# Optimization experiments

Hardware: AMD Instinct MI355X
Metric: run time of the kernel (lower is better)

Reference implementation:

```python
import jax, jax.numpy as jnp
import numpy as np

N_QUBITS = 12
R = 1
EDGES = [(i, (i + 1) % N_QUBITS) for i in range(N_QUBITS)]
DIM = 2 ** N_QUBITS
BATCH = 64
_LET = 'abcdefghijklmnopqrstuvwxy'

_I4 = np.eye(4, dtype=np.float32)
_AD = np.fliplr(_I4).copy()                      # antidiagonal (XX imag pattern)
_YP = np.array([[0,0,0,1],[0,0,-1,0],[0,-1,0,0],[1,0,0,0]], dtype=np.float32)  # YY imag pattern
_CNOT = jnp.asarray(np.array([[1,0,0,0],[0,1,0,0],[0,0,0,1],[0,0,1,0]], dtype=np.complex64))
_k = np.arange(DIM)
# z_signs[i, k] = -1 if bit (n-i-1) of k is set, matching the torch buffer
_ZS = jnp.asarray(np.stack([1.0 - 2.0 * ((_k >> (N_QUBITS - i - 1)) & 1) for i in range(N_QUBITS)]).astype(np.float32))  # [n, 2^n]


def _c(r, i):
    return jax.lax.complex(r, i)


def rx_mat(t):
    c, s, z = jnp.cos(t / 2), jnp.sin(t / 2), jnp.zeros_like(t)
    real = jnp.stack([jnp.stack([c, z], -1), jnp.stack([z, c], -1)], -2)
    imag = jnp.stack([jnp.stack([z, -s], -1), jnp.stack([-s, z], -1)], -2)
    return _c(real, imag)


def ry_mat(t):
    c, s = jnp.cos(t / 2), jnp.sin(t / 2)
    real = jnp.stack([jnp.stack([c, -s], -1), jnp.stack([s, c], -1)], -2)
    return _c(real, jnp.zeros_like(real))


def rz_mat(t):
    p, z = t / 2, jnp.zeros_like(t)
    cp, sp = jnp.cos(p), jnp.sin(p)
    real = jnp.stack([jnp.stack([cp, z], -1), jnp.stack([z, cp], -1)], -2)
    imag = jnp.stack([jnp.stack([-sp, z], -1), jnp.stack([z, sp], -1)], -2)
    return _c(real, imag)


def ising_zz(t):
    p = t / 2
    c, s = jnp.cos(p), jnp.sin(p)
    dr = jnp.stack([c, c, c, c], -1)
    di = jnp.stack([-s, s, s, -s], -1)
    i4 = jnp.asarray(_I4)
    return _c(dr[..., :, None] * i4, di[..., :, None] * i4)


def ising_xx(t):
    c, s = jnp.cos(t / 2), jnp.sin(t / 2)
    return _c(c[..., None, None] * jnp.asarray(_I4), -s[..., None, None] * jnp.asarray(_AD))


def ising_yy(t):
    c, s = jnp.cos(t / 2), jnp.sin(t / 2)
    return _c(c[..., None, None] * jnp.asarray(_I4), s[..., None, None] * jnp.asarray(_YP))


def apply_1q(state, gate, q):
    # state [B, 2^n]; gate [2,2] or [B,2,2]; qubit axis sits at stride 2^q (matches torch view)
    B = state.shape[0]
    left, right = 2 ** (N_QUBITS - q - 1), 2 ** q
    s = state.reshape(B, left, 2, right)
    sub = 'bij' if gate.ndim == 3 else 'ij'
    return jnp.einsum(f'{sub},bljr->blir', gate, s).reshape(B, DIM)


def apply_2q(state, gate, q1, q2):
    # state [B, 2^n]; gate [4,4]; qubit index = tensor-axis index from MSB (matches torch permute path)
    if q1 > q2:
        q1, q2 = q2, q1
    B = state.shape[0]
    s = state.reshape((B,) + (2,) * N_QUBITS)
    g = gate.reshape(2, 2, 2, 2)
    ax = list(_LET[:N_QUBITS])
    out = ax.copy()
    u, v = ax[q1], ax[q2]
    out[q1], out[q2] = 'A', 'B'
    spec = f"AB{u}{v},Z{''.join(ax)}->Z{''.join(out)}"
    return jnp.einsum(spec, g, s).reshape(B, DIM)


def _forward(data, encoding_scale, encoding_bias, eta, ew_zz, ew_xx, ew_yy, nb_z, nb_x, nb_y, trainable_rots):
    B, n = data.shape
    # data-encoding gates, cached once per forward: angles [B, n] -> gates [B, n, 2, 2]
    rx_g = rx_mat(encoding_scale[:, 0] * data + encoding_bias[:, 0])
    ry_g = ry_mat(encoding_scale[:, 1] * data + encoding_bias[:, 1])
    rz_g = rz_mat(encoding_scale[:, 2] * data + encoding_bias[:, 2])
    state = jnp.zeros((B, DIM), jnp.complex64).at[:, 0].set(1.0)
    ising_fns = (ising_zz, ising_xx, ising_yy)
    ews = (ew_zz, ew_xx, ew_yy)
    nbs = (nb_z, nb_x, nb_y)
    bias_fns = (rz_mat, rx_mat, ry_mat)
    enc_types = ('full', 'xy', 'yz')
    for r in range(R):
        for b in range(3):  # blocks: ZZ, XX, YY
            bt = enc_types[b]
            # data encoding
            for q in range(n):
                if bt != 'yz':
                    state = apply_1q(state, rx_g[:, q], q)
                state = apply_1q(state, ry_g[:, q], q)
                if bt != 'xy':
                    state = apply_1q(state, rz_g[:, q], q)
            # Ising interaction on each edge
            theta = eta[r, b] * ews[b][r]            # [n_edges]
            egs = ising_fns[b](theta)                # [n_edges, 4, 4]
            for e, (i, j) in enumerate(EDGES):
                state = apply_2q(state, egs[e], i, j)
            # node biases (RZ / RX / RY matching the block)
            bgs = bias_fns[b](nbs[b][r])             # [n, 2, 2]
            for q in range(n):
                state = apply_1q(state, bgs[q], q)
            # trainable rotations rx, ry, rz per qubit
            rots = trainable_rots[r, b]              # [n, 3]
            rxg, ryg, rzg = rx_mat(rots[:, 0]), ry_mat(rots[:, 1]), rz_mat(rots[:, 2])
            for q in range(n):
                state = apply_1q(state, rxg[q], q)
                state = apply_1q(state, ryg[q], q)
                state = apply_1q(state, rzg[q], q)
            # CNOT entangling ring
            for q in range(n):
                state = apply_2q(state, _CNOT, q, (q + 1) % n)
    probs = state.real ** 2 + state.imag ** 2        # [B, 2^n]
    return probs @ _ZS.T                             # Pauli-Z expectations [B, n]


def setup_inputs() -> dict:
    key = jax.random.key(0)
    ks = jax.random.split(key, 12)
    n, E, f = N_QUBITS, len(EDGES), jnp.float32
    return {
        'data': jax.random.uniform(ks[0], (BATCH, n), f),
        'encoding_scale': jnp.pi * jnp.ones((n, 3), f) + 0.1 * jax.random.normal(ks[1], (n, 3), f),
        'encoding_bias': 0.1 * jax.random.normal(ks[2], (n, 3), f),
        'eta': 0.5 * jnp.ones((R, 3), f),
        'ew_zz': jnp.ones((R, E), f) + 0.1 * jax.random.normal(ks[3], (R, E), f),
        'ew_xx': jnp.ones((R, E), f) + 0.1 * jax.random.normal(ks[4], (R, E), f),
        'ew_yy': jnp.ones((R, E), f) + 0.1 * jax.random.normal(ks[5], (R, E), f),
        'nb_z': 0.1 * jax.random.normal(ks[6], (R, n), f),
        'nb_x': 0.1 * jax.random.normal(ks[7], (R, n), f),
        'nb_y': 0.1 * jax.random.normal(ks[8], (R, n), f),
        'trainable_rots': 0.1 * jax.random.normal(ks[9], (R, 3, n, 3), f),
    }


def reference(data, encoding_scale, encoding_bias, eta, ew_zz, ew_xx, ew_yy, nb_z, nb_x, nb_y, trainable_rots):
    return _forward(data, encoding_scale, encoding_bias, eta, ew_zz, ew_xx, ew_yy, nb_z, nb_x, nb_y, trainable_rots)
```

## Files before the change

kernel.cpp:

```cpp
#include <hip/hip_runtime.h>
#include <math.h>

#define NT 512
#define QDIM 4096

typedef float v2f __attribute__((ext_vector_type(2)));
using F2 = float2;

__device__ __forceinline__ v2f mkv(float x, float y) { v2f r; r.x = x; r.y = y; return r; }

__device__ __forceinline__ v2f cfma(v2f m, v2f a, v2f acc) {
    v2f r;
    asm("v_pk_fma_f32 %0, %1, %2, %3 op_sel:[0,0,0] op_sel_hi:[0,1,1]\n\t"
        "v_pk_fma_f32 %0, %1, %2, %0 op_sel:[1,1,0] op_sel_hi:[1,0,1] neg_lo:[1,0,0]"
        : "=&v"(r) : "v"(m), "v"(a), "v"(acc));
    return r;
}
__device__ __forceinline__ v2f cmulp(v2f m, v2f a) {
    v2f r;
    asm("v_pk_mul_f32 %0, %1, %2 op_sel:[0,0] op_sel_hi:[0,1]\n\t"
        "v_pk_fma_f32 %0, %1, %2, %0 op_sel:[1,1,0] op_sel_hi:[1,0,1] neg_lo:[1,0,0]"
        : "=&v"(r) : "v"(m), "v"(a));
    return r;
}

__device__ __forceinline__ F2 cadd(F2 p, F2 q) { return make_float2(p.x + q.x, p.y + q.y); }
__device__ __forceinline__ F2 cmul(F2 p, F2 q) {
    return make_float2(p.x * q.x - p.y * q.y, p.x * q.y + p.y * q.x);
}
struct M2 { F2 a, b, c, d; };
__device__ __forceinline__ M2 mmul(M2 A, M2 B) {
    M2 R;
    R.a = cadd(cmul(A.a, B.a), cmul(A.b, B.c));
    R.b = cadd(cmul(A.a, B.b), cmul(A.b, B.d));
    R.c = cadd(cmul(A.c, B.a), cmul(A.d, B.c));
    R.d = cadd(cmul(A.c, B.b), cmul(A.d, B.d));
    return R;
}
__device__ __forceinline__ M2 mrx(float t) {
    float s, c; sincosf(0.5f * t, &s, &c);
    return { make_float2(c, 0), make_float2(0, -s), make_float2(0, -s), make_float2(c, 0) };
}
__device__ __forceinline__ M2 mry(float t) {
    float s, c; sincosf(0.5f * t, &s, &c);
    return { make_float2(c, 0), make_float2(-s, 0), make_float2(s, 0), make_float2(c, 0) };
}
__device__ __forceinline__ M2 mrz(float t) {
    float s, c; sincosf(0.5f * t, &s, &c);
    return { make_float2(c, -s), make_float2(0, 0), make_float2(0, 0), make_float2(c, s) };
}
#define RSQ2 0.70710678118654752f
__device__ __forceinline__ M2 mH() {
    return { make_float2(RSQ2, 0), make_float2(RSQ2, 0), make_float2(RSQ2, 0), make_float2(-RSQ2, 0) };
}
__device__ __forceinline__ M2 mW() {
    return { make_float2(RSQ2, 0), make_float2(0, RSQ2), make_float2(RSQ2, 0), make_float2(0, -RSQ2) };
}
__device__ __forceinline__ M2 mWd() {
    return { make_float2(RSQ2, 0), make_float2(RSQ2, 0), make_float2(0, -RSQ2), make_float2(0, RSQ2) };
}


template<int Li>
__device__ __forceinline__ int kOf(int t, int j) {
    const int mlo = (1 << (3 * Li)) - 1;
    return (t & mlo) | (j << (3 * Li)) | ((t & ~mlo) << 3);
}
__device__ __forceinline__ int slot0(int k) {
    int j = k & 7, t = k >> 3;
    return j * 512 + (t ^ j);
}

template<int TYPE>
__device__ __forceinline__ void itrip(v2f* amp, int l, v2f* wb) {
#pragma unroll
    for (int j = 0; j < 8; ++j) wb[j * 64 + (l ^ ((9 * j) & 63))] = amp[j];
    asm volatile("" ::: "memory");
#pragma unroll
    for (int j = 0; j < 8; ++j) {
        int jo, lo;
        if (TYPE == 0) { jo = l & 7;        lo = j | (l & 56); }
        else           { jo = (l >> 3) & 7; lo = (l & 7) | (j << 3); }
        amp[j] = wb[jo * 64 + (lo ^ ((9 * jo) & 63))];
    }
}

__device__ __forceinline__ void btrip(v2f* amp, int tid, int l, int wv, v2f* b) {
#pragma unroll
    for (int j = 0; j < 8; ++j) b[j * 512 + (tid ^ j)] = amp[j];
    __syncthreads();
#pragma unroll
    for (int j = 0; j < 8; ++j) amp[j] = b[wv * 512 + ((j * 64 + l) ^ wv)];
}

struct Trio { v2f m[12]; };
__device__ __forceinline__ Trio load_trio(const float4 (*g4)[2]) {
    Trio t;
#pragma unroll
    for (int k = 0; k < 3; ++k) {
        float4 a = g4[k][0], b = g4[k][1];
        t.m[k * 4 + 0] = mkv(a.x, a.y); t.m[k * 4 + 1] = mkv(a.z, a.w);
        t.m[k * 4 + 2] = mkv(b.x, b.y); t.m[k * 4 + 3] = mkv(b.z, b.w);
    }
    return t;
}

template<int JB>
__device__ __forceinline__ void g1_reg(v2f* amp, const v2f* g) {
    const int m = 1 << JB;
    v2f m00 = g[0], m01 = g[1], m10 = g[2], m11 = g[3];
#pragma unroll
    for (int j = 0; j < 8; ++j)
        if (!(j & m)) {
            v2f a = amp[j], b = amp[j | m];
            amp[j]     = cfma(m01, b, cmulp(m00, a));
            amp[j | m] = cfma(m11, b, cmulp(m10, a));
        }
}
__device__ __forceinline__ void apply_trio(v2f* amp, const Trio& t) {
    g1_reg<0>(amp, t.m + 0);  g1_reg<1>(amp, t.m + 4);  g1_reg<2>(amp, t.m + 8);
}

__device__ __forceinline__ void diag_L3(v2f* amp, const float* zh, int tid) {
    float phi0 = 0.f;
#pragma unroll
    for (int e = 3; e <= 10; ++e) {
        int hi = 11 - e, lo = 10 - e;
        phi0 += (((tid >> hi) ^ (tid >> lo)) & 1) ? zh[e] : -zh[e];
    }
    float z0 = zh[0], z1 = zh[1], z2 = zh[2], z11 = zh[11];
    int t8 = (tid >> 8) & 1, t0 = tid & 1;
#pragma unroll
    for (int j = 0; j < 8; ++j) {
        int j0 = j & 1, j1 = (j >> 1) & 1, j2 = (j >> 2) & 1;
        float phi = phi0
            + ((j2 ^ j1) ? z0 : -z0)
            + ((j1 ^ j0) ? z1 : -z1)
            + ((j0 ^ t8) ? z2 : -z2)
            + ((j2 ^ t0) ? z11 : -z11);
        float sp, cp;
        __sincosf(phi, &sp, &cp);
        amp[j] = cmulp(mkv(cp, sp), amp[j]);
    }
}

__device__ __forceinline__ int cnot_src(int k) {
#pragma unroll
    for (int e = 11; e >= 0; --e) {
        int hi = (e < 11) ? 11 - e : 11, lo = (e < 11) ? 10 - e : 0;
        if ((k >> hi) & 1) k ^= (1 << lo);
    }
    return k;
}

__device__ __forceinline__ void cnot_pair(v2f* amp, int tid, int l, int pw, int gen,
                                          const int* kslot, v2f* b,
                                          volatile unsigned* wflag, int wv) {
#pragma unroll
    for (int j = 0; j < 8; ++j) b[j * 512 + (tid ^ j)] = amp[j];
    asm volatile("" ::: "memory");
    __threadfence_block();
    if (l == 0) wflag[wv] = (unsigned)gen;
    asm volatile("" ::: "memory");
    int guard = 0;
    while (wflag[pw] < (unsigned)gen && guard < (1 << 26)) {
        ++guard;
        __builtin_amdgcn_s_sleep(1);
    }
    asm volatile("" ::: "memory");
#pragma unroll
    for (int j = 0; j < 8; ++j) amp[j] = b[kslot[j]];
}

__global__ __launch_bounds__(NT) void qsim_kernel(
    const float* __restrict__ data,
    const float* __restrict__ enc_scale,
    const float* __restrict__ enc_bias,
    const float* __restrict__ eta,
    const float* __restrict__ ew_zz,
    const float* __restrict__ ew_xx,
    const float* __restrict__ ew_yy,
    const float* __restrict__ nb_z,
    const float* __restrict__ nb_x,
    const float* __restrict__ nb_y,
    const float* __restrict__ trots,
    float* __restrict__ out)
{
    __shared__ v2f bbuf[2][QDIM];
    __shared__ v2f ibuf[QDIM];
    __shared__ float4 g1q4[72][2];
    __shared__ float zhalf[3][12];
    __shared__ float red[8][12];
    __shared__ unsigned wflag[8];

    const int tid = threadIdx.x;
    const int l = tid & 63, wv = tid >> 6;
    const int bat = blockIdx.x;
    v2f* wb = &ibuf[wv * 512];

    if (tid < 36) {
        int b = tid / 12, q = tid % 12;
        float x  = data[bat * 12 + q];
        float ax = enc_scale[q * 3 + 0] * x + enc_bias[q * 3 + 0];
        float ay = enc_scale[q * 3 + 1] * x + enc_bias[q * 3 + 1];
        float az = enc_scale[q * 3 + 2] * x + enc_bias[q * 3 + 2];
        M2 M;
        if (b == 0)      M = mmul(mrz(az), mmul(mry(ay), mrx(ax)));
        else if (b == 1) M = mmul(mH(), mmul(mry(ay), mrx(ax)));
        else             M = mmul(mW(), mmul(mrz(az), mry(ay)));
        g1q4[tid][0] = make_float4(M.a.x, M.a.y, M.b.x, M.b.y);
        g1q4[tid][1] = make_float4(M.c.x, M.c.y, M.d.x, M.d.y);
    } else if (tid < 72) {
        int i = tid - 36, b = i / 12, q = i % 12;
        float nb = (b == 0) ? nb_z[q] : (b == 1) ? nb_x[q] : nb_y[q];
        M2 M0 = (b == 0) ? mrz(nb) : (b == 1) ? mrx(nb) : mry(nb);
        float t0 = trots[(b * 12 + q) * 3 + 0];
        float t1 = trots[(b * 12 + q) * 3 + 1];
        float t2 = trots[(b * 12 + q) * 3 + 2];
        M2 M = mmul(mrz(t2), mmul(mry(t1), mmul(mrx(t0), M0)));
        if (b == 1)      M = mmul(M, mH());
        else if (b == 2) M = mmul(M, mWd());
        g1q4[tid][0] = make_float4(M.a.x, M.a.y, M.b.x, M.b.y);
        g1q4[tid][1] = make_float4(M.c.x, M.c.y, M.d.x, M.d.y);
    } else if (tid < 108) {
        int i = tid - 72, b = i / 12, e = i % 12;
        const float* ew = (b == 0) ? ew_zz : (b == 1) ? ew_xx : ew_yy;
        zhalf[b][e] = 0.5f * eta[b] * ew[e];
    }
    if (tid < 8) wflag[tid] = 0u;
    __syncthreads();

    const int w0 = wv & 1, w1 = (wv >> 1) & 1, w2 = (wv >> 2) & 1;
    const int pw = (w0 ^ w1) | ((w1 ^ w2) << 1) | (w2 << 2);

    int kslot[8];
#pragma unroll
    for (int j = 0; j < 8; ++j)
        kslot[j] = slot0(cnot_src(kOf<0>(tid, j)));

    v2f amp[8];
    int sel = 0;
#define NB (&bbuf[(sel ^= 1) ^ 1][0])

    for (int blk = 0; blk < 3; ++blk) {
        const float4(*Ge)[2] = &g1q4[blk * 12];
        const float4(*Gb)[2] = &g1q4[36 + blk * 12];

        if (blk == 0) {
            v2f base = mkv(1.f, 0.f);
#pragma unroll
            for (int q = 0; q < 9; ++q) {
                float4 r0 = Ge[q][0], r1 = Ge[q][1];
                v2f f = ((tid >> q) & 1) ? mkv(r1.x, r1.y) : mkv(r0.x, r0.y);
                base = cmulp(base, f);
            }
            v2f f9[2], f10[2], f11[2];
            { float4 r0 = Ge[9][0],  r1 = Ge[9][1];  f9[0]  = mkv(r0.x, r0.y); f9[1]  = mkv(r1.x, r1.y); }
            { float4 r0 = Ge[10][0], r1 = Ge[10][1]; f10[0] = mkv(r0.x, r0.y); f10[1] = mkv(r1.x, r1.y); }
            { float4 r0 = Ge[11][0], r1 = Ge[11][1]; f11[0] = mkv(r0.x, r0.y); f11[1] = mkv(r1.x, r1.y); }
#pragma unroll
            for (int j = 0; j < 8; ++j) {
                v2f t = cmulp(f9[j & 1], f10[(j >> 1) & 1]);
                t = cmulp(t, f11[(j >> 2) & 1]);
                amp[j] = cmulp(t, base);
            }
        } else {
            Trio tA = load_trio(Ge + 0);
            apply_trio(amp, tA);
            itrip<0>(amp, l, wb);
            tA = load_trio(Ge + 3);
            apply_trio(amp, tA);
            itrip<1>(amp, l, wb);
            tA = load_trio(Ge + 6);
            apply_trio(amp, tA);
            btrip(amp, tid, l, wv, NB);
            tA = load_trio(Ge + 9);
            apply_trio(amp, tA);
        }

        diag_L3(amp, zhalf[blk], tid);

        Trio tB = load_trio(Gb + 9);
        apply_trio(amp, tB);
        btrip(amp, tid, l, wv, NB);
        tB = load_trio(Gb + 6);
        apply_trio(amp, tB);
        itrip<1>(amp, l, wb);
        tB = load_trio(Gb + 3);
        apply_trio(amp, tB);
        itrip<0>(amp, l, wb);
        tB = load_trio(Gb + 0);
        apply_trio(amp, tB);

        cnot_pair(amp, tid, l, pw, blk + 1, kslot, NB, wflag, wv);
    }

    float pr[8];
#pragma unroll
    for (int j = 0; j < 8; ++j) pr[j] = amp[j].x * amp[j].x + amp[j].y * amp[j].y;
    float psum = 0.f;
#pragma unroll
    for (int j = 0; j < 8; ++j) psum += pr[j];

    float acc[12];
#pragma unroll
    for (int i = 0; i < 9; ++i)
        acc[i] = ((tid >> (8 - i)) & 1) ? -psum : psum;
#pragma unroll
    for (int i = 9; i < 12; ++i) {
        float s = 0.f;
        int bit = 11 - i;
#pragma unroll
        for (int j = 0; j < 8; ++j)
            s += ((j >> bit) & 1) ? -pr[j] : pr[j];
        acc[i] = s;
    }
#pragma unroll
    for (int off = 32; off > 0; off >>= 1)
#pragma unroll
        for (int i = 0; i < 12; ++i)
            acc[i] += __shfl_down(acc[i], off, 64);
    if (l == 0)
#pragma unroll
        for (int i = 0; i < 12; ++i) red[wv][i] = acc[i];
    __syncthreads();
    if (tid < 12) {
        float s = 0.f;
#pragma unroll
        for (int ww = 0; ww < 8; ++ww) s += red[ww][tid];
        out[bat * 12 + tid] = s;
    }
}

extern "C" void kernel_launch(void* const* d_in, const int* in_sizes, int n_in,
                              void* d_out, int out_size, void* d_ws, size_t ws_size,
                              hipStream_t stream) {
    const float* data      = (const float*)d_in[0];
    const float* enc_scale = (const float*)d_in[1];
    const float* enc_bias  = (const float*)d_in[2];
    const float* eta       = (const float*)d_in[3];
    const float* ew_zz     = (const float*)d_in[4];
    const float* ew_xx     = (const float*)d_in[5];
    const float* ew_yy     = (const float*)d_in[6];
    const float* nb_z      = (const float*)d_in[7];
    const float* nb_x      = (const float*)d_in[8];
    const float* nb_y      = (const float*)d_in[9];
    const float* trots     = (const float*)d_in[10];
    float* out = (float*)d_out;

    int batch = out_size / 12;
    qsim_kernel<<<batch, NT, 0, stream>>>(data, enc_scale, enc_bias, eta,
                                          ew_zz, ew_xx, ew_yy,
                                          nb_z, nb_x, nb_y, trots, out);
}
```

Baseline: 91.30 us.

## Switch to 16 amplitudes per thread with 256-thread blocks and 4-qubit register groups

The state-vector kernel now holds 16 amplitudes per thread instead of 8 and uses 256 threads per block. Single-qubit gates are applied in groups of four qubits in registers rather than three. That cuts the number of LDS transposes per layer and halves the warps taking part in the barrier and flag syncs. The cost is higher register pressure and fewer threads per block, which may lower latency hiding when only 64 blocks exist.

```diff
diff --git a/kernel.cpp b/kernel.cpp
--- a/kernel.cpp
+++ b/kernel.cpp
@@ -1,7 +1,7 @@
 #include <hip/hip_runtime.h>
 #include <math.h>
 
-#define NT 512
+#define NT 256
 #define QDIM 4096
 
 typedef float v2f __attribute__((ext_vector_type(2)));
@@ -61,43 +61,46 @@
 }
 
 
-template<int Li>
-__device__ __forceinline__ int kOf(int t, int j) {
-    const int mlo = (1 << (3 * Li)) - 1;
-    return (t & mlo) | (j << (3 * Li)) | ((t & ~mlo) << 3);
-}
-__device__ __forceinline__ int slot0(int k) {
-    int j = k & 7, t = k >> 3;
-    return j * 512 + (t ^ j);
-}
-
-template<int TYPE>
-__device__ __forceinline__ void itrip(v2f* amp, int l, v2f* wb) {
-#pragma unroll
-    for (int j = 0; j < 8; ++j) wb[j * 64 + (l ^ ((9 * j) & 63))] = amp[j];
+__device__ __forceinline__ int bslot(int k) {
+    int hi = k >> 6;
+    return (hi << 6) | ((k & 63) ^ hi);
+}
+
+__device__ __forceinline__ void itrip01(v2f* amp, int l, v2f* wb) {
+#pragma unroll
+    for (int j = 0; j < 16; ++j) wb[(j << 6) | (l ^ j)] = amp[j];
     asm volatile("" ::: "memory");
 #pragma unroll
-    for (int j = 0; j < 8; ++j) {
-        int jo, lo;
-        if (TYPE == 0) { jo = l & 7;        lo = j | (l & 56); }
-        else           { jo = (l >> 3) & 7; lo = (l & 7) | (j << 3); }
-        amp[j] = wb[jo * 64 + (lo ^ ((9 * jo) & 63))];
-    }
-}
-
-__device__ __forceinline__ void btrip(v2f* amp, int tid, int l, int wv, v2f* b) {
-#pragma unroll
-    for (int j = 0; j < 8; ++j) b[j * 512 + (tid ^ j)] = amp[j];
+    for (int j = 0; j < 16; ++j) {
+        int jo = l & 15, lo = j | (l & 48);
+        amp[j] = wb[(jo << 6) | (lo ^ jo)];
+    }
+}
+
+__device__ __forceinline__ void btrip12(v2f* amp, int l, int wv, v2f* b) {
+#pragma unroll
+    for (int j = 0; j < 16; ++j)
+        b[bslot((l & 15) | (j << 4) | ((l >> 4) << 8) | (wv << 10))] = amp[j];
     __syncthreads();
 #pragma unroll
-    for (int j = 0; j < 8; ++j) amp[j] = b[wv * 512 + ((j * 64 + l) ^ wv)];
-}
-
-struct Trio { v2f m[12]; };
-__device__ __forceinline__ Trio load_trio(const float4 (*g4)[2]) {
-    Trio t;
-#pragma unroll
-    for (int k = 0; k < 3; ++k) {
+    for (int j = 0; j < 16; ++j)
+        amp[j] = b[bslot(l | (wv << 6) | (j << 8))];
+}
+__device__ __forceinline__ void btrip21(v2f* amp, int l, int wv, v2f* b) {
+#pragma unroll
+    for (int j = 0; j < 16; ++j)
+        b[bslot(l | (wv << 6) | (j << 8))] = amp[j];
+    __syncthreads();
+#pragma unroll
+    for (int j = 0; j < 16; ++j)
+        amp[j] = b[bslot((l & 15) | (j << 4) | ((l >> 4) << 8) | (wv << 10))];
+}
+
+struct Quad { v2f m[16]; };
+__device__ __forceinline__ Quad load_quad(const float4 (*g4)[2]) {
+    Quad t;
+#pragma unroll
+    for (int k = 0; k < 4; ++k) {
         float4 a = g4[k][0], b = g4[k][1];
         t.m[k * 4 + 0] = mkv(a.x, a.y); t.m[k * 4 + 1] = mkv(a.z, a.w);
         t.m[k * 4 + 2] = mkv(b.x, b.y); t.m[k * 4 + 3] = mkv(b.z, b.w);
@@ -110,34 +113,36 @@
     const int m = 1 << JB;
     v2f m00 = g[0], m01 = g[1], m10 = g[2], m11 = g[3];
 #pragma unroll
-    for (int j = 0; j < 8; ++j)
+    for (int j = 0; j < 16; ++j)
         if (!(j & m)) {
             v2f a = amp[j], b = amp[j | m];
             amp[j]     = cfma(m01, b, cmulp(m00, a));
             amp[j | m] = cfma(m11, b, cmulp(m10, a));
         }
 }
-__device__ __forceinline__ void apply_trio(v2f* amp, const Trio& t) {
-    g1_reg<0>(amp, t.m + 0);  g1_reg<1>(amp, t.m + 4);  g1_reg<2>(amp, t.m + 8);
-}
-
-__device__ __forceinline__ void diag_L3(v2f* amp, const float* zh, int tid) {
+__device__ __forceinline__ void apply_quad(v2f* amp, const Quad& t) {
+    g1_reg<0>(amp, t.m + 0);  g1_reg<1>(amp, t.m + 4);
+    g1_reg<2>(amp, t.m + 8);  g1_reg<3>(amp, t.m + 12);
+}
+
+__device__ __forceinline__ void diag_L2(v2f* amp, const float* zh, int T) {
     float phi0 = 0.f;
 #pragma unroll
-    for (int e = 3; e <= 10; ++e) {
+    for (int e = 4; e <= 10; ++e) {
         int hi = 11 - e, lo = 10 - e;
-        phi0 += (((tid >> hi) ^ (tid >> lo)) & 1) ? zh[e] : -zh[e];
-    }
-    float z0 = zh[0], z1 = zh[1], z2 = zh[2], z11 = zh[11];
-    int t8 = (tid >> 8) & 1, t0 = tid & 1;
-#pragma unroll
-    for (int j = 0; j < 8; ++j) {
-        int j0 = j & 1, j1 = (j >> 1) & 1, j2 = (j >> 2) & 1;
+        phi0 += (((T >> hi) ^ (T >> lo)) & 1) ? zh[e] : -zh[e];
+    }
+    float z0 = zh[0], z1 = zh[1], z2 = zh[2], z3 = zh[3], z11 = zh[11];
+    int t7 = (T >> 7) & 1, t0 = T & 1;
+#pragma unroll
+    for (int j = 0; j < 16; ++j) {
+        int j0 = j & 1, j1 = (j >> 1) & 1, j2 = (j >> 2) & 1, j3 = (j >> 3) & 1;
         float phi = phi0
-            + ((j2 ^ j1) ? z0 : -z0)
-            + ((j1 ^ j0) ? z1 : -z1)
-            + ((j0 ^ t8) ? z2 : -z2)
-            + ((j2 ^ t0) ? z11 : -z11);
+            + ((j3 ^ j2) ? z0 : -z0)
+            + ((j2 ^ j1) ? z1 : -z1)
+            + ((j1 ^ j0) ? z2 : -z2)
+            + ((j0 ^ t7) ? z3 : -z3)
+            + ((j3 ^ t0) ? z11 : -z11);
         float sp, cp;
         __sincosf(phi, &sp, &cp);
         amp[j] = cmulp(mkv(cp, sp), amp[j]);
@@ -153,11 +158,12 @@
     return k;
 }
 
-__device__ __forceinline__ void cnot_pair(v2f* amp, int tid, int l, int pw, int gen,
+__device__ __forceinline__ void cnot_pair(v2f* amp, int l, int wv, int pw, int gen,
                                           const int* kslot, v2f* b,
-                                          volatile unsigned* wflag, int wv) {
-#pragma unroll
-    for (int j = 0; j < 8; ++j) b[j * 512 + (tid ^ j)] = amp[j];
+                                          volatile unsigned* wflag) {
+#pragma unroll
+    for (int j = 0; j < 16; ++j)
+        b[bslot(j | (l << 4) | (wv << 10))] = amp[j];
     asm volatile("" ::: "memory");
     __threadfence_block();
     if (l == 0) wflag[wv] = (unsigned)gen;
@@ -169,7 +175,7 @@
     }
     asm volatile("" ::: "memory");
 #pragma unroll
-    for (int j = 0; j < 8; ++j) amp[j] = b[kslot[j]];
+    for (int j = 0; j < 16; ++j) amp[j] = b[kslot[j]];
 }
 
 __global__ __launch_bounds__(NT) void qsim_kernel(
@@ -190,13 +196,13 @@
     __shared__ v2f ibuf[QDIM];
     __shared__ float4 g1q4[72][2];
     __shared__ float zhalf[3][12];
-    __shared__ float red[8][12];
-    __shared__ unsigned wflag[8];
+    __shared__ float red[4][12];
+    __shared__ unsigned wflag[4];
 
     const int tid = threadIdx.x;
     const int l = tid & 63, wv = tid >> 6;
     const int bat = blockIdx.x;
-    v2f* wb = &ibuf[wv * 512];
+    v2f* wb = &ibuf[wv << 10];
 
     if (tid < 36) {
         int b = tid / 12, q = tid % 12;
@@ -227,18 +233,19 @@
         const float* ew = (b == 0) ? ew_zz : (b == 1) ? ew_xx : ew_yy;
         zhalf[b][e] = 0.5f * eta[b] * ew[e];
     }
-    if (tid < 8) wflag[tid] = 0u;
+    if (tid < 4) wflag[tid] = 0u;
     __syncthreads();
 
-    const int w0 = wv & 1, w1 = (wv >> 1) & 1, w2 = (wv >> 2) & 1;
-    const int pw = (w0 ^ w1) | ((w1 ^ w2) << 1) | (w2 << 2);
-
-    int kslot[8];
-#pragma unroll
-    for (int j = 0; j < 8; ++j)
-        kslot[j] = slot0(cnot_src(kOf<0>(tid, j)));
-
-    v2f amp[8];
+    const int w0 = wv & 1, w1 = (wv >> 1) & 1;
+    const int pw = (w0 ^ w1) | (w1 << 1);
+    const int T = l | (wv << 6);
+
+    int kslot[16];
+#pragma unroll
+    for (int j = 0; j < 16; ++j)
+        kslot[j] = bslot(cnot_src(j | (l << 4) | (wv << 10)));
+
+    v2f amp[16];
     int sel = 0;
 #define NB (&bbuf[(sel ^= 1) ^ 1][0])
 
@@ -249,69 +256,67 @@
         if (blk == 0) {
             v2f base = mkv(1.f, 0.f);
 #pragma unroll
-            for (int q = 0; q < 9; ++q) {
+            for (int q = 0; q < 8; ++q) {
                 float4 r0 = Ge[q][0], r1 = Ge[q][1];
-                v2f f = ((tid >> q) & 1) ? mkv(r1.x, r1.y) : mkv(r0.x, r0.y);
+                v2f f = ((T >> q) & 1) ? mkv(r1.x, r1.y) : mkv(r0.x, r0.y);
                 base = cmulp(base, f);
             }
-            v2f f9[2], f10[2], f11[2];
+            v2f f8[2], f9[2], f10[2], f11[2];
+            { float4 r0 = Ge[8][0],  r1 = Ge[8][1];  f8[0]  = mkv(r0.x, r0.y); f8[1]  = mkv(r1.x, r1.y); }
             { float4 r0 = Ge[9][0],  r1 = Ge[9][1];  f9[0]  = mkv(r0.x, r0.y); f9[1]  = mkv(r1.x, r1.y); }
             { float4 r0 = Ge[10][0], r1 = Ge[10][1]; f10[0] = mkv(r0.x, r0.y); f10[1] = mkv(r1.x, r1.y); }
             { float4 r0 = Ge[11][0], r1 = Ge[11][1]; f11[0] = mkv(r0.x, r0.y); f11[1] = mkv(r1.x, r1.y); }
-#pragma unroll
-            for (int j = 0; j < 8; ++j) {
-                v2f t = cmulp(f9[j & 1], f10[(j >> 1) & 1]);
-                t = cmulp(t, f11[(j >> 2) & 1]);
-                amp[j] = cmulp(t, base);
+            v2f g01[4], g23[4];
+#pragma unroll
+            for (int a = 0; a < 4; ++a) {
+                g01[a] = cmulp(f8[a & 1], f9[(a >> 1) & 1]);
+                g23[a] = cmulp(cmulp(f10[a & 1], f11[(a >> 1) & 1]), base);
             }
+#pragma unroll
+            for (int j = 0; j < 16; ++j)
+                amp[j] = cmulp(g01[j & 3], g23[j >> 2]);
         } else {
-            Trio tA = load_trio(Ge + 0);
-            apply_trio(amp, tA);
-            itrip<0>(amp, l, wb);
-            tA = load_trio(Ge + 3);
-            apply_trio(amp, tA);
-            itrip<1>(amp, l, wb);
-            tA = load_trio(Ge + 6);
-            apply_trio(amp, tA);
-            btrip(amp, tid, l, wv, NB);
-            tA = load_trio(Ge + 9);
-            apply_trio(amp, tA);
+            Quad tA = load_quad(Ge + 0);
+            apply_quad(amp, tA);
+            itrip01(amp, l, wb);
+            tA = load_quad(Ge + 4);
+            apply_quad(amp, tA);
+            btrip12(amp, l, wv, NB);
+            tA = load_quad(Ge + 8);
+            apply_quad(amp, tA);
         }
 
-        diag_L3(amp, zhalf[blk], tid);
-
-        Trio tB = load_trio(Gb + 9);
-        apply_trio(amp, tB);
-        btrip(amp, tid, l, wv, NB);
-        tB = load_trio(Gb + 6);
-        apply_trio(amp, tB);
-        itrip<1>(amp, l, wb);
-        tB = load_trio(Gb + 3);
-        apply_trio(amp, tB);
-        itrip<0>(amp, l, wb);
-        tB = load_trio(Gb + 0);
-        apply_trio(amp, tB);
-
-        cnot_pair(amp, tid, l, pw, blk + 1, kslot, NB, wflag, wv);
-    }
-
-    float pr[8];
-#pragma unroll
-    for (int j = 0; j < 8; ++j) pr[j] = amp[j].x * amp[j].x + amp[j].y * amp[j].y;
+        diag_L2(amp, zhalf[blk], T);
+
+        Quad tB = load_quad(Gb + 8);
+        apply_quad(amp, tB);
+        btrip21(amp, l, wv, NB);
+        tB = load_quad(Gb + 4);
+        apply_quad(amp, tB);
+        itrip01(amp, l, wb);
+        tB = load_quad(Gb + 0);
+        apply_quad(amp, tB);
+
+        cnot_pair(amp, l, wv, pw, blk + 1, kslot, NB, wflag);
+    }
+
+    float pr[16];
+#pragma unroll
+    for (int j = 0; j < 16; ++j) pr[j] = amp[j].x * amp[j].x + amp[j].y * amp[j].y;
     float psum = 0.f;
 #pragma unroll
-    for (int j = 0; j < 8; ++j) psum += pr[j];
+    for (int j = 0; j < 16; ++j) psum += pr[j];
 
     float acc[12];
 #pragma unroll
-    for (int i = 0; i < 9; ++i)
-        acc[i] = ((tid >> (8 - i)) & 1) ? -psum : psum;
-#pragma unroll
-    for (int i = 9; i < 12; ++i) {
+    for (int i = 0; i < 8; ++i)
+        acc[i] = ((T >> (7 - i)) & 1) ? -psum : psum;
+#pragma unroll
+    for (int i = 8; i < 12; ++i) {
         float s = 0.f;
         int bit = 11 - i;
 #pragma unroll
-        for (int j = 0; j < 8; ++j)
+        for (int j = 0; j < 16; ++j)
             s += ((j >> bit) & 1) ? -pr[j] : pr[j];
         acc[i] = s;
     }
@@ -327,7 +332,7 @@
     if (tid < 12) {
         float s = 0.f;
 #pragma unroll
-        for (int ww = 0; ww < 8; ++ww) s += red[ww][tid];
+        for (int ww = 0; ww < 4; ++ww) s += red[ww][tid];
         out[bat * 12 + tid] = s;
     }
 }
```

New measurement: 95.26 us. 4.3% more time.
